# Performance work log

Measured on AMD Instinct MI355X. Metric: run time of the kernel, lower is better.

The kernel has to match this reference:

```python
import jax, jax.numpy as jnp
import numpy as np

N_USERS = 100_000
N_ITEMS = 50_000
N_NODES = N_USERS + N_ITEMS
EMBED_DIM = 64
N_LAYERS = 3
N_INTERACTIONS = 1_600_000
BATCH = 4096


def setup_inputs() -> dict:
    key = jax.random.key(0)
    k_u, k_i, k_eu, k_ei, k_bu, k_bp, k_bn = jax.random.split(key, 7)

    # Xavier-uniform embeddings: bound = sqrt(6 / (fan_in + fan_out))
    bu = float(np.sqrt(6.0 / (N_USERS + EMBED_DIM)))
    bi = float(np.sqrt(6.0 / (N_ITEMS + EMBED_DIM)))
    user_emb = jax.random.uniform(k_u, (N_USERS, EMBED_DIM), jnp.float32, -bu, bu)
    item_emb = jax.random.uniform(k_i, (N_ITEMS, EMBED_DIM), jnp.float32, -bi, bi)

    # Random bipartite interactions, symmetrized: edges (u, N_USERS+i) and (N_USERS+i, u)
    eu = np.asarray(jax.random.randint(k_eu, (N_INTERACTIONS,), 0, N_USERS), dtype=np.int32)
    ei = np.asarray(jax.random.randint(k_ei, (N_INTERACTIONS,), 0, N_ITEMS), dtype=np.int32) + N_USERS
    row = np.concatenate([eu, ei])  # [E]
    col = np.concatenate([ei, eu])  # [E]

    # Symmetric normalization D^-1/2 A D^-1/2 (standard LightGCN graph)
    deg = np.bincount(row, minlength=N_NODES).astype(np.float32)
    deg = np.maximum(deg, 1.0)
    d_inv_sqrt = 1.0 / np.sqrt(deg)
    vals = (d_inv_sqrt[row] * d_inv_sqrt[col]).astype(np.float32)  # [E]

    users = jax.random.randint(k_bu, (BATCH,), 0, N_USERS, dtype=jnp.int32)
    pos_items = jax.random.randint(k_bp, (BATCH,), 0, N_ITEMS, dtype=jnp.int32)
    neg_items = jax.random.randint(k_bn, (BATCH,), 0, N_ITEMS, dtype=jnp.int32)

    return {
        "user_emb": user_emb,
        "item_emb": item_emb,
        "row": jnp.asarray(row),
        "col": jnp.asarray(col),
        "vals": jnp.asarray(vals),
        "users": users,
        "pos_items": pos_items,
        "neg_items": neg_items,
    }


def _spmm(row, col, vals, x):
    # sparse @ x via gather + weighted segment-sum, [E, D] intermediate
    return jax.ops.segment_sum(vals[:, None] * x[col], row, num_segments=N_NODES)


def reference(user_emb, item_emb, row, col, vals, users, pos_items, neg_items):
    all_emb = jnp.concatenate([user_emb, item_emb], axis=0)  # [N, D]
    # running mean over (n_layers + 1) propagation stages
    acc = all_emb
    for _ in range(N_LAYERS):
        all_emb = _spmm(row, col, vals, all_emb)
        acc = acc + all_emb
    light_out = acc / (N_LAYERS + 1)
    final_users = light_out[:N_USERS]
    final_items = light_out[N_USERS:]
    return (final_users[users], final_items[pos_items], final_items[neg_items])
```

## Files before the change

### kernel.cpp

```cpp
#include <hip/hip_runtime.h>

#define EMBED 64
#define BSHIFT 9
#define BROWS 512
#define NGROUPS 256
#define PTHREADS 1024
#define MAXNB 512
#define SCAN_THREADS 256
#define SCAN_ITEMS 16
#define SCAN_TILE (SCAN_THREADS * SCAN_ITEMS)

typedef unsigned short ushort_t;
typedef __attribute__((ext_vector_type(2))) float f32x2;

__device__ __forceinline__ ushort_t f2bf(float f) {
    unsigned u = __float_as_uint(f);
    return (ushort_t)((u + 0x7FFFu + ((u >> 16) & 1u)) >> 16);
}
__device__ __forceinline__ float bf2f(ushort_t b) {
    return __uint_as_float(((unsigned)b) << 16);
}

__global__ void scan_tiles(const int* __restrict__ in, int* __restrict__ out,
                           int* __restrict__ tile_sums, int n) {
    __shared__ int sh[SCAN_THREADS];
    int t = threadIdx.x;
    int base = blockIdx.x * SCAN_TILE + t * SCAN_ITEMS;
    int vals[SCAN_ITEMS];
    int sum = 0;
#pragma unroll
    for (int k = 0; k < SCAN_ITEMS; ++k) {
        int idx = base + k;
        vals[k] = (idx < n) ? in[idx] : 0;
        sum += vals[k];
    }
    sh[t] = sum;
    __syncthreads();
    for (int off = 1; off < SCAN_THREADS; off <<= 1) {
        int v = (t >= off) ? sh[t - off] : 0;
        __syncthreads();
        sh[t] += v;
        __syncthreads();
    }
    int excl = sh[t] - sum;
    if (t == SCAN_THREADS - 1) tile_sums[blockIdx.x] = sh[t];
    int run = excl;
#pragma unroll
    for (int k = 0; k < SCAN_ITEMS; ++k) {
        int idx = base + k;
        if (idx < n) out[idx] = run;
        run += vals[k];
    }
}

__global__ void add_bases_f(int* __restrict__ arr, const int* __restrict__ tile_sums,
                            int n, int ntiles) {
    int i = blockIdx.x * blockDim.x + threadIdx.x;
    if (i >= n) {
        if (i == n) {
            int s = 0;
            for (int j = 0; j < ntiles; ++j) s += tile_sums[j];
            arr[n] = s;
        }
        return;
    }
    int myt = i / SCAN_TILE;
    int base = 0;
    for (int j = 0; j < myt; ++j) base += tile_sums[j];
    arr[i] += base;
}

__global__ __launch_bounds__(PTHREADS) void passA_hist(const int* __restrict__ row,
                                                       int* __restrict__ cnt,
                                                       int nnz, int nb, int epb) {
    __shared__ int hist[MAXNB];
    int g = blockIdx.x, t = threadIdx.x;
    for (int b = t; b < nb; b += PTHREADS) hist[b] = 0;
    __syncthreads();
    int i0 = g * epb, i1 = min(i0 + epb, nnz);
    for (int i = i0 + t; i < i1; i += PTHREADS) atomicAdd(&hist[row[i] >> BSHIFT], 1);
    __syncthreads();
    for (int b = t; b < nb; b += PTHREADS) cnt[b * NGROUPS + g] = hist[b];
}

__global__ __launch_bounds__(PTHREADS) void passB_scatter(const int* __restrict__ row,
                                                          const int* __restrict__ col,
                                                          const int* __restrict__ cbase,
                                                          int* __restrict__ tpack,
                                                          int nnz, int nb, int epb) {
    __shared__ int lcur[MAXNB];
    int g = blockIdx.x, t = threadIdx.x;
    for (int b = t; b < nb; b += PTHREADS) lcur[b] = cbase[b * NGROUPS + g];
    __syncthreads();
    int i0 = g * epb, i1 = min(i0 + epb, nnz);
    for (int i = i0 + t; i < i1; i += PTHREADS) {
        int r = row[i];
        int slot = atomicAdd(&lcur[r >> BSHIFT], 1);
        tpack[slot] = ((r & (BROWS - 1)) << 20) | col[i];
    }
}

__global__ __launch_bounds__(PTHREADS) void build_bucket(const int* __restrict__ cbase,
                                                         const int* __restrict__ tpack,
                                                         const float* __restrict__ ue,
                                                         const float* __restrict__ ie,
                                                         int* __restrict__ deg,
                                                         float* __restrict__ dinv,
                                                         int* __restrict__ offs,
                                                         int* __restrict__ eoff,
                                                         ushort_t* __restrict__ xa,
                                                         ushort_t* __restrict__ xb,
                                                         ushort_t* __restrict__ xc,
                                                         int n_nodes, int n_users, int nnz) {
    __shared__ int hist[BROWS];
    __shared__ int sscan[BROWS];
    __shared__ int lcur[BROWS];
    __shared__ float sdinv[BROWS];
    int b = blockIdx.x, t = threadIdx.x;
    int r0 = b * BROWS;
    int r1 = min(r0 + BROWS, n_nodes);
    for (int r = t; r < BROWS; r += PTHREADS) hist[r] = 0;
    __syncthreads();
    int es = cbase[b * NGROUPS];
    int ee = cbase[(b + 1) * NGROUPS];
    for (int e = es + t; e < ee; e += PTHREADS) atomicAdd(&hist[((unsigned)tpack[e]) >> 20], 1);
    __syncthreads();
    if (t < BROWS) sscan[t] = hist[t];
    __syncthreads();
    for (int off = 1; off < BROWS; off <<= 1) {
        int v = 0;
        if (t < BROWS && t >= off) v = sscan[t - off];
        __syncthreads();
        if (t < BROWS) sscan[t] += v;
        __syncthreads();
    }
    if (t < BROWS) {
        int d = hist[t];
        int excl = es + sscan[t] - d;
        lcur[t] = excl;
        if (t < r1 - r0) {
            deg[r0 + t] = d;
            float di = 1.0f / sqrtf((float)max(d, 1));
            dinv[r0 + t] = di;
            sdinv[t] = di;
            offs[r0 + t] = excl;
        }
    }
    if (b == 0 && t == 0) offs[n_nodes] = nnz;
    __syncthreads();
    for (int e = es + t; e < ee; e += PTHREADS) {
        int pk = tpack[e];
        int slot = atomicAdd(&lcur[((unsigned)pk) >> 20], 1);
        eoff[slot] = (pk & 0xFFFFF) << 7;
    }
    int nq = (r1 - r0) * 16;
    for (int idx = t; idx < nq; idx += PTHREADS) {
        int rl = idx >> 4, q = idx & 15;
        int grow = r0 + rl;
        const float* src = (grow < n_users) ? (ue + (size_t)grow * EMBED)
                                            : (ie + (size_t)(grow - n_users) * EMBED);
        float4 v = ((const float4*)src)[q];
        float d = sdinv[rl];
        ushort4 o;
        o.x = f2bf(d * v.x); o.y = f2bf(d * v.y); o.z = f2bf(d * v.z); o.w = f2bf(d * v.w);
        ((ushort4*)(xa + (size_t)grow * EMBED))[q] = o;
    }
    if (b == 0 && t < 48) {
        ushort4 z = {0, 0, 0, 0};
        ushort_t* tgt = (t < 16) ? xa : ((t < 32) ? xb : xc);
        ((ushort4*)(tgt + (size_t)n_nodes * EMBED))[t & 15] = z;
    }
}

__global__ __launch_bounds__(256, 8) void spmm_bf16(const int* __restrict__ offs,
                                                    const int* __restrict__ eoff,
                                                    const float* __restrict__ dinv,
                                                    const ushort_t* __restrict__ x,
                                                    ushort_t* __restrict__ y, int n_nodes) {
    int wave = blockIdx.x * (blockDim.x >> 6) + (threadIdx.x >> 6);
    int lane = threadIdx.x & 63;
    int g = lane >> 3;
    int l8 = lane & 7;
    int row = wave * 8 + g;
    bool valid = row < n_nodes;
    int start = valid ? offs[row] : 0;
    int end = valid ? offs[row + 1] : 0;
    int maxdeg = end - start;
#pragma unroll
    for (int m = 1; m < 64; m <<= 1) maxdeg = max(maxdeg, __shfl_xor(maxdeg, m));
    int pad = n_nodes << 7;
    const char* xb = (const char*)x + (l8 << 4);
    f32x2 a0 = 0.f, a1 = 0.f, a2 = 0.f, a3 = 0.f;
#define GATH(K)                                                                           \
    {                                                                                     \
        int cc = __shfl(c_lane, (g << 3) + K);                                            \
        uint4 q = *(const uint4*)(xb + cc);                                               \
        a0 += (f32x2){__uint_as_float(q.x << 16), __uint_as_float(q.x & 0xFFFF0000u)};    \
        a1 += (f32x2){__uint_as_float(q.y << 16), __uint_as_float(q.y & 0xFFFF0000u)};    \
        a2 += (f32x2){__uint_as_float(q.z << 16), __uint_as_float(q.z & 0xFFFF0000u)};    \
        a3 += (f32x2){__uint_as_float(q.w << 16), __uint_as_float(q.w & 0xFFFF0000u)};    \
    }
    for (int k0 = 0; k0 < maxdeg; k0 += 8) {
        int il = start + k0 + l8;
        int c_lane = (il < end) ? eoff[il] : pad;
        int nk = maxdeg - k0;
        if (nk > 8) nk = 8;
        switch (nk) {
            case 8: GATH(7); [[fallthrough]];
            case 7: GATH(6); [[fallthrough]];
            case 6: GATH(5); [[fallthrough]];
            case 5: GATH(4); [[fallthrough]];
            case 4: GATH(3); [[fallthrough]];
            case 3: GATH(2); [[fallthrough]];
            case 2: GATH(1); [[fallthrough]];
            case 1: GATH(0);
        }
    }
#undef GATH
    if (valid) {
        float dr = dinv[row];
        float s = dr * dr;
        uint4 o;
        o.x = (unsigned)f2bf(s * a0.x) | ((unsigned)f2bf(s * a0.y) << 16);
        o.y = (unsigned)f2bf(s * a1.x) | ((unsigned)f2bf(s * a1.y) << 16);
        o.z = (unsigned)f2bf(s * a2.x) | ((unsigned)f2bf(s * a2.y) << 16);
        o.w = (unsigned)f2bf(s * a3.x) | ((unsigned)f2bf(s * a3.y) << 16);
        *(uint4*)(y + (size_t)row * EMBED + l8 * 8) = o;
    }
}

__global__ __launch_bounds__(256, 8) void gather_sel(const int* __restrict__ offs,
                                                     const int* __restrict__ eoff,
                                                     const float* __restrict__ dinv,
                                                     const float* __restrict__ ue,
                                                     const float* __restrict__ ie,
                                                     const ushort_t* __restrict__ x1,
                                                     const ushort_t* __restrict__ x2,
                                                     const int* __restrict__ users,
                                                     const int* __restrict__ pos,
                                                     const int* __restrict__ neg,
                                                     float* __restrict__ out,
                                                     int batch, int n_users, int n_nodes) {
    int w = blockIdx.x * (blockDim.x >> 6) + (threadIdx.x >> 6);
    int total = 3 * batch;
    if (w >= total) return;
    int lane = threadIdx.x & 63;
    int g = lane >> 3;
    int l8 = lane & 7;
    int which = w / batch;
    int b = w - which * batch;
    int node;
    const float* e0p;
    if (which == 0) {
        int u = users[b];
        node = u;
        e0p = ue + (size_t)u * EMBED;
    } else {
        int it = (which == 1) ? pos[b] : neg[b];
        node = n_users + it;
        e0p = ie + (size_t)it * EMBED;
    }
    int start = offs[node];
    int end = offs[node + 1];
    int pad = n_nodes << 7;
    const char* xb = (const char*)x2 + (l8 << 4);
    f32x2 a0 = 0.f, a1 = 0.f, a2 = 0.f, a3 = 0.f;
#define GATH(K)                                                                           \
    {                                                                                     \
        int cc = __shfl(c_lane, (K << 3) + g);                                            \
        uint4 q = *(const uint4*)(xb + cc);                                               \
        a0 += (f32x2){__uint_as_float(q.x << 16), __uint_as_float(q.x & 0xFFFF0000u)};    \
        a1 += (f32x2){__uint_as_float(q.y << 16), __uint_as_float(q.y & 0xFFFF0000u)};    \
        a2 += (f32x2){__uint_as_float(q.z << 16), __uint_as_float(q.z & 0xFFFF0000u)};    \
        a3 += (f32x2){__uint_as_float(q.w << 16), __uint_as_float(q.w & 0xFFFF0000u)};    \
    }
    for (int base = start; base < end; base += 64) {
        int m = end - base;
        if (m > 64) m = 64;
        int il = base + lane;
        int c_lane = (il < end) ? eoff[il] : pad;
        int nk = (m + 7) >> 3;
        switch (nk) {
            case 8: GATH(7); [[fallthrough]];
            case 7: GATH(6); [[fallthrough]];
            case 6: GATH(5); [[fallthrough]];
            case 5: GATH(4); [[fallthrough]];
            case 4: GATH(3); [[fallthrough]];
            case 3: GATH(2); [[fallthrough]];
            case 2: GATH(1); [[fallthrough]];
            case 1: GATH(0);
        }
    }
#undef GATH
    float r0 = a0.x, r1 = a0.y, r2 = a1.x, r3 = a1.y;
    float r4 = a2.x, r5 = a2.y, r6 = a3.x, r7 = a3.y;
#pragma unroll
    for (int msk = 8; msk <= 32; msk <<= 1) {
        r0 += __shfl_xor(r0, msk);
        r1 += __shfl_xor(r1, msk);
        r2 += __shfl_xor(r2, msk);
        r3 += __shfl_xor(r3, msk);
        r4 += __shfl_xor(r4, msk);
        r5 += __shfl_xor(r5, msk);
        r6 += __shfl_xor(r6, msk);
        r7 += __shfl_xor(r7, msk);
    }
    if (g == 0) {
        float dr = dinv[node];
        float sd = 1.0f / dr;
        size_t xoff = (size_t)node * EMBED + l8 * 8;
        uint4 q1 = *(const uint4*)(x1 + xoff);
        uint4 q2 = *(const uint4*)(x2 + xoff);
        float4 e0a = *(const float4*)(e0p + l8 * 8);
        float4 e0b = *(const float4*)(e0p + l8 * 8 + 4);
        float l12_0 = bf2f((ushort_t)(q1.x & 0xFFFF)) + bf2f((ushort_t)(q2.x & 0xFFFF));
        float l12_1 = bf2f((ushort_t)(q1.x >> 16)) + bf2f((ushort_t)(q2.x >> 16));
        float l12_2 = bf2f((ushort_t)(q1.y & 0xFFFF)) + bf2f((ushort_t)(q2.y & 0xFFFF));
        float l12_3 = bf2f((ushort_t)(q1.y >> 16)) + bf2f((ushort_t)(q2.y >> 16));
        float l12_4 = bf2f((ushort_t)(q1.z & 0xFFFF)) + bf2f((ushort_t)(q2.z & 0xFFFF));
        float l12_5 = bf2f((ushort_t)(q1.z >> 16)) + bf2f((ushort_t)(q2.z >> 16));
        float l12_6 = bf2f((ushort_t)(q1.w & 0xFFFF)) + bf2f((ushort_t)(q2.w & 0xFFFF));
        float l12_7 = bf2f((ushort_t)(q1.w >> 16)) + bf2f((ushort_t)(q2.w >> 16));
        float* op = out + (size_t)w * EMBED + l8 * 8;
        float4 o0, o1;
        o0.x = 0.25f * (e0a.x + sd * l12_0 + dr * r0);
        o0.y = 0.25f * (e0a.y + sd * l12_1 + dr * r1);
        o0.z = 0.25f * (e0a.z + sd * l12_2 + dr * r2);
        o0.w = 0.25f * (e0a.w + sd * l12_3 + dr * r3);
        o1.x = 0.25f * (e0b.x + sd * l12_4 + dr * r4);
        o1.y = 0.25f * (e0b.y + sd * l12_5 + dr * r5);
        o1.z = 0.25f * (e0b.z + sd * l12_6 + dr * r6);
        o1.w = 0.25f * (e0b.w + sd * l12_7 + dr * r7);
        *(float4*)op = o0;
        *(float4*)(op + 4) = o1;
    }
}

extern "C" void kernel_launch(void* const* d_in, const int* in_sizes, int n_in,
                              void* d_out, int out_size, void* d_ws, size_t ws_size,
                              hipStream_t stream) {
    const float* user_emb = (const float*)d_in[0];
    const float* item_emb = (const float*)d_in[1];
    const int* row = (const int*)d_in[2];
    const int* col = (const int*)d_in[3];
    const int* users = (const int*)d_in[5];
    const int* pos = (const int*)d_in[6];
    const int* neg = (const int*)d_in[7];
    float* out = (float*)d_out;

    int n_users = in_sizes[0] / EMBED;
    int n_items = in_sizes[1] / EMBED;
    int n_nodes = n_users + n_items;
    int nnz = in_sizes[2];
    int batch = in_sizes[5];
    int nb = (n_nodes + BROWS - 1) / BROWS;
    int n2 = nb * NGROUPS;
    int epb = (nnz + NGROUPS - 1) / NGROUPS;

    char* p = (char*)d_ws;
    auto alloc = [&](size_t bytes) -> void* {
        void* r = (void*)p;
        p += (bytes + 255) & ~(size_t)255;
        return r;
    };
    int ntiles2 = (n2 + SCAN_TILE - 1) / SCAN_TILE;
    int* deg = (int*)alloc(sizeof(int) * (size_t)n_nodes);
    int* offs = (int*)alloc(sizeof(int) * (size_t)(n_nodes + 1));
    float* dinv = (float*)alloc(sizeof(float) * (size_t)n_nodes);
    int* cnt = (int*)alloc(sizeof(int) * (size_t)n2);
    int* cbase = (int*)alloc(sizeof(int) * (size_t)(n2 + 1));
    int* tile_sums = (int*)alloc(sizeof(int) * (size_t)ntiles2);
    int* eoff = (int*)alloc(sizeof(int) * ((size_t)nnz + 64));
    ushort_t* bufA = (ushort_t*)alloc(sizeof(ushort_t) * (size_t)(n_nodes + 1) * EMBED);
    ushort_t* bufB = (ushort_t*)alloc(sizeof(ushort_t) * (size_t)(n_nodes + 1) * EMBED);
    ushort_t* bufC = (ushort_t*)alloc(sizeof(ushort_t) * (size_t)(n_nodes + 1) * EMBED);
    if ((size_t)(p - (char*)d_ws) > ws_size) return;
    int* tpack = (int*)bufB;

    passA_hist<<<NGROUPS, PTHREADS, 0, stream>>>(row, cnt, nnz, nb, epb);
    scan_tiles<<<ntiles2, SCAN_THREADS, 0, stream>>>(cnt, cbase, tile_sums, n2);
    add_bases_f<<<(n2 + 256) / 256, 256, 0, stream>>>(cbase, tile_sums, n2, ntiles2);
    passB_scatter<<<NGROUPS, PTHREADS, 0, stream>>>(row, col, cbase, tpack, nnz, nb, epb);
    build_bucket<<<nb, PTHREADS, 0, stream>>>(cbase, tpack, user_emb, item_emb, deg, dinv,
                                              offs, eoff, bufA, bufB, bufC, n_nodes,
                                              n_users, nnz);

    int waves = (n_nodes + 7) / 8;
    int spmm_blocks = (waves + 3) / 4;
    spmm_bf16<<<spmm_blocks, 256, 0, stream>>>(offs, eoff, dinv, bufA, bufB, n_nodes);
    spmm_bf16<<<spmm_blocks, 256, 0, stream>>>(offs, eoff, dinv, bufB, bufC, n_nodes);

    int selw = 3 * batch;
    gather_sel<<<(selw + 3) / 4, 256, 0, stream>>>(offs, eoff, dinv, user_emb, item_emb,
                                                   bufB, bufC, users, pos, neg, out,
                                                   batch, n_users, n_nodes);
}
```

Measured before the change: 205.4 us.

## Sort rows by degree so each SpMM wave processes similar-degree rows

```diff
diff --git a/kernel.cpp b/kernel.cpp
--- a/kernel.cpp
+++ b/kernel.cpp
@@ -6,6 +6,7 @@
 #define NGROUPS 256
 #define PTHREADS 1024
 #define MAXNB 512
+#define NCLS 512
 #define SCAN_THREADS 256
 #define SCAN_ITEMS 16
 #define SCAN_TILE (SCAN_THREADS * SCAN_ITEMS)
@@ -108,18 +109,22 @@
                                                          float* __restrict__ dinv,
                                                          int* __restrict__ offs,
                                                          int* __restrict__ eoff,
+                                                         int* __restrict__ dcnt,
                                                          ushort_t* __restrict__ xa,
                                                          ushort_t* __restrict__ xb,
                                                          ushort_t* __restrict__ xc,
-                                                         int n_nodes, int n_users, int nnz) {
+                                                         int n_nodes, int n_users, int nnz,
+                                                         int nb) {
     __shared__ int hist[BROWS];
     __shared__ int sscan[BROWS];
     __shared__ int lcur[BROWS];
+    __shared__ int chist[NCLS];
     __shared__ float sdinv[BROWS];
     int b = blockIdx.x, t = threadIdx.x;
     int r0 = b * BROWS;
     int r1 = min(r0 + BROWS, n_nodes);
     for (int r = t; r < BROWS; r += PTHREADS) hist[r] = 0;
+    for (int c = t; c < NCLS; c += PTHREADS) chist[c] = 0;
     __syncthreads();
     int es = cbase[b * NGROUPS];
     int ee = cbase[(b + 1) * NGROUPS];
@@ -144,10 +149,12 @@
             dinv[r0 + t] = di;
             sdinv[t] = di;
             offs[r0 + t] = excl;
+            atomicAdd(&chist[min(d, NCLS - 1)], 1);
         }
     }
     if (b == 0 && t == 0) offs[n_nodes] = nnz;
     __syncthreads();
+    for (int c = t; c < NCLS; c += PTHREADS) dcnt[c * nb + b] = chist[c];
     for (int e = es + t; e < ee; e += PTHREADS) {
         int pk = tpack[e];
         int slot = atomicAdd(&lcur[((unsigned)pk) >> 20], 1);
@@ -172,8 +179,27 @@
     }
 }
 
+__global__ __launch_bounds__(PTHREADS) void perm_scatter(const int* __restrict__ deg,
+                                                         const int* __restrict__ dbase,
+                                                         int* __restrict__ perm,
+                                                         int n_nodes, int nb) {
+    __shared__ int cur[NCLS];
+    int b = blockIdx.x, t = threadIdx.x;
+    int r0 = b * BROWS;
+    int r1 = min(r0 + BROWS, n_nodes);
+    if (r0 >= n_nodes) return;
+    for (int c = t; c < NCLS; c += PTHREADS) cur[c] = dbase[c * nb + b];
+    __syncthreads();
+    for (int r = r0 + t; r < r1; r += PTHREADS) {
+        int cls = min(deg[r], NCLS - 1);
+        int slot = atomicAdd(&cur[cls], 1);
+        perm[slot] = r;
+    }
+}
+
 __global__ __launch_bounds__(256, 8) void spmm_bf16(const int* __restrict__ offs,
                                                     const int* __restrict__ eoff,
+                                                    const int* __restrict__ perm,
                                                     const float* __restrict__ dinv,
                                                     const ushort_t* __restrict__ x,
                                                     ushort_t* __restrict__ y, int n_nodes) {
@@ -181,8 +207,9 @@
     int lane = threadIdx.x & 63;
     int g = lane >> 3;
     int l8 = lane & 7;
-    int row = wave * 8 + g;
-    bool valid = row < n_nodes;
+    int idx = wave * 8 + g;
+    bool valid = idx < n_nodes;
+    int row = valid ? perm[idx] : 0;
     int start = valid ? offs[row] : 0;
     int end = valid ? offs[row + 1] : 0;
     int maxdeg = end - start;
@@ -355,6 +382,7 @@
     int batch = in_sizes[5];
     int nb = (n_nodes + BROWS - 1) / BROWS;
     int n2 = nb * NGROUPS;
+    int n3 = nb * NCLS;
     int epb = (nnz + NGROUPS - 1) / NGROUPS;
 
     char* p = (char*)d_ws;
@@ -364,12 +392,17 @@
         return r;
     };
     int ntiles2 = (n2 + SCAN_TILE - 1) / SCAN_TILE;
+    int ntiles3 = (n3 + SCAN_TILE - 1) / SCAN_TILE;
+    int ntiles_max = ntiles2 > ntiles3 ? ntiles2 : ntiles3;
     int* deg = (int*)alloc(sizeof(int) * (size_t)n_nodes);
     int* offs = (int*)alloc(sizeof(int) * (size_t)(n_nodes + 1));
     float* dinv = (float*)alloc(sizeof(float) * (size_t)n_nodes);
+    int* perm = (int*)alloc(sizeof(int) * ((size_t)n_nodes + 8));
     int* cnt = (int*)alloc(sizeof(int) * (size_t)n2);
     int* cbase = (int*)alloc(sizeof(int) * (size_t)(n2 + 1));
-    int* tile_sums = (int*)alloc(sizeof(int) * (size_t)ntiles2);
+    int* dcnt = (int*)alloc(sizeof(int) * (size_t)n3);
+    int* dbase = (int*)alloc(sizeof(int) * (size_t)(n3 + 1));
+    int* tile_sums = (int*)alloc(sizeof(int) * (size_t)ntiles_max);
     int* eoff = (int*)alloc(sizeof(int) * ((size_t)nnz + 64));
     ushort_t* bufA = (ushort_t*)alloc(sizeof(ushort_t) * (size_t)(n_nodes + 1) * EMBED);
     ushort_t* bufB = (ushort_t*)alloc(sizeof(ushort_t) * (size_t)(n_nodes + 1) * EMBED);
@@ -382,13 +415,16 @@
     add_bases_f<<<(n2 + 256) / 256, 256, 0, stream>>>(cbase, tile_sums, n2, ntiles2);
     passB_scatter<<<NGROUPS, PTHREADS, 0, stream>>>(row, col, cbase, tpack, nnz, nb, epb);
     build_bucket<<<nb, PTHREADS, 0, stream>>>(cbase, tpack, user_emb, item_emb, deg, dinv,
-                                              offs, eoff, bufA, bufB, bufC, n_nodes,
-                                              n_users, nnz);
+                                              offs, eoff, dcnt, bufA, bufB, bufC, n_nodes,
+                                              n_users, nnz, nb);
+    scan_tiles<<<ntiles3, SCAN_THREADS, 0, stream>>>(dcnt, dbase, tile_sums, n3);
+    add_bases_f<<<(n3 + 256) / 256, 256, 0, stream>>>(dbase, tile_sums, n3, ntiles3);
+    perm_scatter<<<nb, PTHREADS, 0, stream>>>(deg, dbase, perm, n_nodes, nb);
 
     int waves = (n_nodes + 7) / 8;
     int spmm_blocks = (waves + 3) / 4;
-    spmm_bf16<<<spmm_blocks, 256, 0, stream>>>(offs, eoff, dinv, bufA, bufB, n_nodes);
-    spmm_bf16<<<spmm_blocks, 256, 0, stream>>>(offs, eoff, dinv, bufB, bufC, n_nodes);
+    spmm_bf16<<<spmm_blocks, 256, 0, stream>>>(offs, eoff, perm, dinv, bufA, bufB, n_nodes);
+    spmm_bf16<<<spmm_blocks, 256, 0, stream>>>(offs, eoff, perm, dinv, bufB, bufC, n_nodes);
 
     int selw = 3 * batch;
     gather_sel<<<(selw + 3) / 4, 256, 0, stream>>>(offs, eoff, dinv, user_emb, item_emb,
```

Measured after the change: 229.1 us. +11.6%, slower.

## Sort rows by degree within each bucket to balance SpMM wave work

Applied to the files above, without the earlier changes.

```diff
diff --git a/kernel.cpp b/kernel.cpp
--- a/kernel.cpp
+++ b/kernel.cpp
@@ -6,6 +6,7 @@
 #define NGROUPS 256
 #define PTHREADS 1024
 #define MAXNB 512
+#define NCLS 512
 #define SCAN_THREADS 256
 #define SCAN_ITEMS 16
 #define SCAN_TILE (SCAN_THREADS * SCAN_ITEMS)
@@ -108,6 +109,7 @@
                                                          float* __restrict__ dinv,
                                                          int* __restrict__ offs,
                                                          int* __restrict__ eoff,
+                                                         int* __restrict__ perm,
                                                          ushort_t* __restrict__ xa,
                                                          ushort_t* __restrict__ xb,
                                                          ushort_t* __restrict__ xc,
@@ -115,17 +117,23 @@
     __shared__ int hist[BROWS];
     __shared__ int sscan[BROWS];
     __shared__ int lcur[BROWS];
+    __shared__ int ccur[NCLS];
     __shared__ float sdinv[BROWS];
     int b = blockIdx.x, t = threadIdx.x;
     int r0 = b * BROWS;
     int r1 = min(r0 + BROWS, n_nodes);
+    int nrows = r1 - r0;
     for (int r = t; r < BROWS; r += PTHREADS) hist[r] = 0;
+    for (int c = t; c < NCLS; c += PTHREADS) ccur[c] = 0;
     __syncthreads();
     int es = cbase[b * NGROUPS];
     int ee = cbase[(b + 1) * NGROUPS];
     for (int e = es + t; e < ee; e += PTHREADS) atomicAdd(&hist[((unsigned)tpack[e]) >> 20], 1);
     __syncthreads();
-    if (t < BROWS) sscan[t] = hist[t];
+    if (t < BROWS) {
+        sscan[t] = hist[t];
+        if (t < nrows) atomicAdd(&ccur[min(hist[t], NCLS - 1)], 1);
+    }
     __syncthreads();
     for (int off = 1; off < BROWS; off <<= 1) {
         int v = 0;
@@ -138,7 +146,7 @@
         int d = hist[t];
         int excl = es + sscan[t] - d;
         lcur[t] = excl;
-        if (t < r1 - r0) {
+        if (t < nrows) {
             deg[r0 + t] = d;
             float di = 1.0f / sqrtf((float)max(d, 1));
             dinv[r0 + t] = di;
@@ -148,12 +156,28 @@
     }
     if (b == 0 && t == 0) offs[n_nodes] = nnz;
     __syncthreads();
+    if (t < NCLS) sscan[t] = ccur[t];
+    __syncthreads();
+    for (int off = 1; off < NCLS; off <<= 1) {
+        int v = 0;
+        if (t < NCLS && t >= off) v = sscan[t - off];
+        __syncthreads();
+        if (t < NCLS) sscan[t] += v;
+        __syncthreads();
+    }
+    if (t < NCLS) ccur[t] = sscan[t] - ccur[t];
+    __syncthreads();
+    if (t < nrows) {
+        int cls = min(hist[t], NCLS - 1);
+        int slot = atomicAdd(&ccur[cls], 1);
+        perm[r0 + slot] = r0 + t;
+    }
     for (int e = es + t; e < ee; e += PTHREADS) {
         int pk = tpack[e];
         int slot = atomicAdd(&lcur[((unsigned)pk) >> 20], 1);
         eoff[slot] = (pk & 0xFFFFF) << 7;
     }
-    int nq = (r1 - r0) * 16;
+    int nq = nrows * 16;
     for (int idx = t; idx < nq; idx += PTHREADS) {
         int rl = idx >> 4, q = idx & 15;
         int grow = r0 + rl;
@@ -174,6 +198,7 @@
 
 __global__ __launch_bounds__(256, 8) void spmm_bf16(const int* __restrict__ offs,
                                                     const int* __restrict__ eoff,
+                                                    const int* __restrict__ perm,
                                                     const float* __restrict__ dinv,
                                                     const ushort_t* __restrict__ x,
                                                     ushort_t* __restrict__ y, int n_nodes) {
@@ -181,8 +206,9 @@
     int lane = threadIdx.x & 63;
     int g = lane >> 3;
     int l8 = lane & 7;
-    int row = wave * 8 + g;
-    bool valid = row < n_nodes;
+    int idx = wave * 8 + g;
+    bool valid = idx < n_nodes;
+    int row = valid ? perm[idx] : 0;
     int start = valid ? offs[row] : 0;
     int end = valid ? offs[row + 1] : 0;
     int maxdeg = end - start;
@@ -367,6 +393,7 @@
     int* deg = (int*)alloc(sizeof(int) * (size_t)n_nodes);
     int* offs = (int*)alloc(sizeof(int) * (size_t)(n_nodes + 1));
     float* dinv = (float*)alloc(sizeof(float) * (size_t)n_nodes);
+    int* perm = (int*)alloc(sizeof(int) * ((size_t)n_nodes + 8));
     int* cnt = (int*)alloc(sizeof(int) * (size_t)n2);
     int* cbase = (int*)alloc(sizeof(int) * (size_t)(n2 + 1));
     int* tile_sums = (int*)alloc(sizeof(int) * (size_t)ntiles2);
@@ -382,13 +409,13 @@
     add_bases_f<<<(n2 + 256) / 256, 256, 0, stream>>>(cbase, tile_sums, n2, ntiles2);
     passB_scatter<<<NGROUPS, PTHREADS, 0, stream>>>(row, col, cbase, tpack, nnz, nb, epb);
     build_bucket<<<nb, PTHREADS, 0, stream>>>(cbase, tpack, user_emb, item_emb, deg, dinv,
-                                              offs, eoff, bufA, bufB, bufC, n_nodes,
+                                              offs, eoff, perm, bufA, bufB, bufC, n_nodes,
                                               n_users, nnz);
 
     int waves = (n_nodes + 7) / 8;
     int spmm_blocks = (waves + 3) / 4;
-    spmm_bf16<<<spmm_blocks, 256, 0, stream>>>(offs, eoff, dinv, bufA, bufB, n_nodes);
-    spmm_bf16<<<spmm_blocks, 256, 0, stream>>>(offs, eoff, dinv, bufB, bufC, n_nodes);
+    spmm_bf16<<<spmm_blocks, 256, 0, stream>>>(offs, eoff, perm, dinv, bufA, bufB, n_nodes);
+    spmm_bf16<<<spmm_blocks, 256, 0, stream>>>(offs, eoff, perm, dinv, bufB, bufC, n_nodes);
 
     int selw = 3 * batch;
     gather_sel<<<(selw + 3) / 4, 256, 0, stream>>>(offs, eoff, dinv, user_emb, item_emb,
```

New measurement: 225.0 us. 1.1x slower.
